# Performance work log

Measured on AMD Instinct MI355X. Metric: run time of the kernel, lower is better.

Reference implementation:

```python
import jax, jax.numpy as jnp
import numpy as np

N = 50000          # nodes
E = 400000         # edges
MUL0 = 16          # multiplicity of 0e irreps (node & message)
MUL1 = 8           # multiplicity of 1o irreps
RBF = 8
HID = 64
CUTOFF = 5.0
WNUM = MUL0*MUL0 + MUL1*MUL0 + MUL0*MUL1 + MUL1*MUL1  # 576 tp weights per edge
EPS = 1e-8
INV_SQRT3 = 1.0 / np.sqrt(3.0).astype(np.float32)
A_PATH = 1.0 / np.sqrt(float(MUL0 + MUL1))  # e3nn path normalization (fan_in = 24 for both outputs)


def _split_sv(x):
    # x: [n, 40] -> scalars [n,16], vectors [n,8,3]
    return x[:, :MUL0], x[:, MUL0:].reshape(-1, MUL1, 3)


def _irrep_norm(x):
    # RMS-normalize each irrep block separately (IrrepNorm)
    s, v = _split_sv(x)
    s_rms = jnp.sqrt(jnp.mean(s * s, axis=-1, keepdims=True) + EPS)
    v_rms = jnp.sqrt(jnp.mean(jnp.sum(v * v, axis=-1), axis=-1, keepdims=True) + EPS)
    return jnp.concatenate([s / s_rms, (v / v_rms[:, :, None]).reshape(-1, MUL1 * 3)], axis=-1)


def setup_inputs() -> dict:
    key = jax.random.key(0)
    ks = jax.random.split(key, 20)
    inp = {
        'x': jax.random.normal(ks[0], (N, MUL0 + 3 * MUL1), jnp.float32),
        'edge_src': jax.random.randint(ks[1], (E,), 0, N, jnp.int32),
        'edge_dst': jax.random.randint(ks[2], (E,), 0, N, jnp.int32),
        'edge_sh': jax.random.normal(ks[3], (E, 4), jnp.float32),
        'edge_rbf': jax.random.uniform(ks[4], (E, RBF), jnp.float32),
        'edge_len': jax.random.uniform(ks[5], (E,), jnp.float32) * CUTOFF,
        # radial MLP producing per-edge TP weights
        'w_r1': jax.random.normal(ks[6], (RBF, HID), jnp.float32) / np.sqrt(RBF),
        'b_r1': jnp.zeros((HID,), jnp.float32),
        'w_r2': jax.random.normal(ks[7], (HID, WNUM), jnp.float32) / np.sqrt(HID),
        'b_r2': jnp.zeros((WNUM,), jnp.float32),
        # edge gate MLP
        'w_g1': jax.random.normal(ks[8], (RBF, HID), jnp.float32) / np.sqrt(RBF),
        'b_g1': jnp.zeros((HID,), jnp.float32),
        'w_g2': jax.random.normal(ks[9], (HID, 1), jnp.float32) / np.sqrt(HID),
        'b_g2': jnp.zeros((1,), jnp.float32),
        # msg_linear: 16x0e+8x1o -> (16x0e scalars + 8x0e gates) + 8x1o gated
        'Wm_s': jax.random.normal(ks[10], (MUL0, MUL0 + MUL1), jnp.float32),
        'Wm_v': jax.random.normal(ks[11], (MUL1, MUL1), jnp.float32),
        # update_linear and self_linear: 16x0e+8x1o -> 16x0e+8x1o
        'Wu_s': jax.random.normal(ks[12], (MUL0, MUL0), jnp.float32),
        'Wu_v': jax.random.normal(ks[13], (MUL1, MUL1), jnp.float32),
        'Ws_s': jax.random.normal(ks[14], (MUL0, MUL0), jnp.float32),
        'Ws_v': jax.random.normal(ks[15], (MUL1, MUL1), jnp.float32),
        'res_scale': jnp.asarray(0.1, jnp.float32),
    }
    return inp


def reference(x, edge_src, edge_dst, edge_sh, edge_rbf, edge_len,
              w_r1, b_r1, w_r2, b_r2, w_g1, b_g1, w_g2, b_g2,
              Wm_s, Wm_v, Wu_s, Wu_v, Ws_s, Ws_v, res_scale):
    x_norm = _irrep_norm(x)
    xs, xv = _split_sv(x_norm)

    # per-edge TP weights from radial MLP
    w = jax.nn.silu(edge_rbf @ w_r1 + b_r1) @ w_r2 + b_r2            # [E, 576]
    o = MUL0 * MUL0
    w1 = w[:, :o].reshape(-1, MUL0, MUL0)                            # 0e x 0e -> 0e
    w2 = w[:, o:o + MUL1 * MUL0].reshape(-1, MUL1, MUL0)             # 1o x 1o -> 0e
    o += MUL1 * MUL0
    w3 = w[:, o:o + MUL0 * MUL1].reshape(-1, MUL0, MUL1)             # 0e x 1o -> 1o
    o += MUL0 * MUL1
    w4 = w[:, o:].reshape(-1, MUL1, MUL1)                            # 1o x 0e -> 1o

    # gather per-edge source features
    s_e = xs[edge_src]                                               # [E,16]
    v_e = xv[edge_src]                                               # [E,8,3]
    sh0 = edge_sh[:, :1]                                             # [E,1]
    sh1 = edge_sh[:, 1:4]                                            # [E,3]

    # fully-connected tensor product (CG for l<=1, component norm, path norm)
    m0 = A_PATH * (jnp.einsum('ei,eij->ej', s_e * sh0, w1)
                   + INV_SQRT3 * jnp.einsum('eic,ec,eij->ej', v_e, sh1, w2))   # [E,16]
    m1 = A_PATH * (jnp.einsum('ei,eij,ec->ejc', s_e, w3, sh1)
                   + jnp.einsum('eic,eij->ejc', v_e * sh0[:, :, None], w4))    # [E,8,3]

    # cutoff and sigmoid edge gate
    cw = 0.5 * (jnp.cos(jnp.pi * edge_len / CUTOFF) + 1.0) * (edge_len < CUTOFF)
    gw = jax.nn.sigmoid(jax.nn.silu(edge_rbf @ w_g1 + b_g1) @ w_g2 + b_g2)     # [E,1]
    ew = cw[:, None] * gw                                                      # [E,1]
    m0 = m0 * ew
    m1 = m1 * ew[:, :, None]

    # scatter-add into destination nodes, normalize by total edge weight
    agg0 = jax.ops.segment_sum(m0, edge_dst, num_segments=N)                   # [N,16]
    agg1 = jax.ops.segment_sum(m1.reshape(-1, MUL1 * 3), edge_dst, num_segments=N).reshape(-1, MUL1, 3)
    norm = jax.ops.segment_sum(ew, edge_dst, num_segments=N)                   # [N,1]
    norm = jnp.maximum(norm, EPS)
    agg0 = agg0 / norm
    agg1 = agg1 / norm[:, :, None]

    # msg_linear (equivariant linear, fan-in normalized)
    sc = agg0 @ Wm_s / np.sqrt(MUL0)                                           # [N,24]
    vv = jnp.einsum('nic,ij->njc', agg1, Wm_v) / np.sqrt(MUL1)                 # [N,8,3]

    # gated nonlinearity
    scal = jax.nn.silu(sc[:, :MUL0])
    gates = jax.nn.sigmoid(sc[:, MUL0:])
    vg = vv * gates[:, :, None]

    # update + self interaction, residual
    out_s = scal @ Wu_s / np.sqrt(MUL0) + xs @ Ws_s / np.sqrt(MUL0)
    out_v = (jnp.einsum('nic,ij->njc', vg, Wu_v) + jnp.einsum('nic,ij->njc', xv, Ws_v)) / np.sqrt(MUL1)
    out = jnp.concatenate([out_s, out_v.reshape(-1, MUL1 * 3)], axis=-1)
    return x + res_scale * out
```

## Files before the change

### kernel.cpp

```cpp
#include <hip/hip_runtime.h>
#include <cstdint>

#define MUL0 16
#define MUL1 8
#define NRBF 8
#define HID 64
#define WNUM 576
#define CUTOFF 5.0f
#define EPSF 1e-8f

#define INV_SQRT3 0.57735026918962576f
#define A_PATH    0.20412414523193154f
#define Q16       0.25f
#define Q8        0.35355339059327373f
#define PI_OVER_CUT 0.62831853071795865f

typedef _Float16 f16;
typedef _Float16 f16x8 __attribute__((ext_vector_type(8)));
typedef float f32x4 __attribute__((ext_vector_type(4)));

__device__ __forceinline__ float sigm(float x) { return 1.0f / (1.0f + __expf(-x)); }

extern "C" __global__ __launch_bounds__(256) void k_prep_w2t(
    const float* __restrict__ w_r2, f16* __restrict__ W2T) {
  int t = blockIdx.x * 256 + threadIdx.x;
  if (t >= HID * WNUM) return;
  int n = t >> 6, k = t & 63;
  W2T[n * 64 + k] = (f16)w_r2[k * WNUM + n];
}

extern "C" __global__ __launch_bounds__(256) void k_xnorm(
    const float* __restrict__ x, float* __restrict__ xnorm, int N) {
  int n = blockIdx.x * 256 + threadIdx.x;
  if (n >= N) return;
  const float4* xr = (const float4*)(x + (long long)n * 40);
  float4 vv[10];
#pragma unroll
  for (int i = 0; i < 10; i++) vv[i] = xr[i];
  float* f = (float*)vv;
  float ss = 0.f, vs = 0.f;
#pragma unroll
  for (int i = 0; i < 16; i++) ss += f[i] * f[i];
#pragma unroll
  for (int i = 16; i < 40; i++) vs += f[i] * f[i];
  float sr = rsqrtf(ss * (1.0f / 16.0f) + EPSF);
  float vr = rsqrtf(vs * (1.0f / 8.0f) + EPSF);
#pragma unroll
  for (int i = 0; i < 16; i++) f[i] *= sr;
#pragma unroll
  for (int i = 16; i < 40; i++) f[i] *= vr;
  float4* o = (float4*)(xnorm + (long long)n * 40);
#pragma unroll
  for (int i = 0; i < 10; i++) o[i] = vv[i];
}

extern "C" __global__ __launch_bounds__(256, 5) void k_edge(
    const float* __restrict__ xnorm, const int* __restrict__ esrc,
    const int* __restrict__ edst, const float* __restrict__ sh,
    const float* __restrict__ rbf, const float* __restrict__ elen,
    const float* __restrict__ w_r1, const float* __restrict__ b_r1,
    const float* __restrict__ w_g1, const float* __restrict__ b_g1,
    const float* __restrict__ w_g2, const float* __restrict__ b_g2,
    const float* __restrict__ b_r2, const f16* __restrict__ W2T,
    float* __restrict__ agg0, float* __restrict__ agg1,
    float* __restrict__ normb, int E) {
  __shared__ __align__(16) f16   s_H[4][16][72];
  __shared__ __align__(16) float s_sn[4][16][20];
  __shared__ __align__(16) float s_v[4][16][28];
  __shared__ __align__(16) float s_a1[4][16][12];
  __shared__ __align__(16) float s_sh[4][16][4];
  __shared__ __align__(16) float s_rbf[4][16][8];
  __shared__ float s_ew[4][16];
  __shared__ int   s_dst[4][16];

  const int t = threadIdx.x;
  const int w = t >> 6;
  const int lane = t & 63;
  const long long eb = (long long)blockIdx.x * 64 + w * 16;

  const int ge_l = lane >> 2;
  const int part = lane & 3;
  const long long ge = eb + ge_l;
  int srcn = 0;
  float4 shv = {0.f, 0.f, 0.f, 0.f};
  if (ge < E) {
    srcn = esrc[ge];
    shv = *(const float4*)&sh[ge * 4];
  }
  {
    long long gb = eb * 8 + lane;
    float r0 = (gb < (long long)E * 8) ? rbf[gb] : 0.f;
    float r1 = (gb + 64 < (long long)E * 8) ? rbf[gb + 64] : 0.f;
    (&s_rbf[w][0][0])[lane] = r0;
    (&s_rbf[w][0][0])[lane + 64] = r1;
    long long gs = eb * 4 + lane;
    (&s_sh[w][0][0])[lane] = (gs < (long long)E * 4) ? sh[gs] : 0.f;
    if (lane < 16) {
      long long g2 = eb + lane;
      s_dst[w][lane] = (g2 < E) ? edst[g2] : 0;
    }
  }
  __syncthreads();

  {
    const float* xr = xnorm + (long long)srcn * 40;
    if (part < 2) {
      float4 aLo = *(const float4*)(xr + part * 8);
      float4 aHi = *(const float4*)(xr + part * 8 + 4);
      *(float4*)&s_sn[w][ge_l][part * 8] = aLo;
      *(float4*)&s_sn[w][ge_l][part * 8 + 4] = aHi;
    } else {
      const int i0 = (part - 2) * 4;
      const float* vp = xr + 16 + i0 * 3;
      float4 v0 = *(const float4*)(vp);
      float4 v1 = *(const float4*)(vp + 4);
      float4 v2 = *(const float4*)(vp + 8);
      *(float4*)&s_v[w][ge_l][i0 * 3] = v0;
      *(float4*)&s_v[w][ge_l][i0 * 3 + 4] = v1;
      *(float4*)&s_v[w][ge_l][i0 * 3 + 8] = v2;
      float s1x = shv.y, s1y = shv.z, s1z = shv.w;
      s_a1[w][ge_l][i0]     = INV_SQRT3 * (v0.x * s1x + v0.y * s1y + v0.z * s1z);
      s_a1[w][ge_l][i0 + 1] = INV_SQRT3 * (v0.w * s1x + v1.x * s1y + v1.y * s1z);
      s_a1[w][ge_l][i0 + 2] = INV_SQRT3 * (v1.z * s1x + v1.w * s1y + v2.x * s1z);
      s_a1[w][ge_l][i0 + 3] = INV_SQRT3 * (v2.y * s1x + v2.z * s1y + v2.w * s1z);
    }
  }

  {
    float wr[8];
#pragma unroll
    for (int r = 0; r < 8; r++) wr[r] = w_r1[r * HID + lane];
    float bh = b_r1[lane];
#pragma unroll
    for (int u = 0; u < 16; u++) {
      float4 ra = *(const float4*)&s_rbf[w][u][0];
      float4 rb = *(const float4*)&s_rbf[w][u][4];
      float acc = bh + ra.x * wr[0] + ra.y * wr[1] + ra.z * wr[2] + ra.w * wr[3]
                     + rb.x * wr[4] + rb.y * wr[5] + rb.z * wr[6] + rb.w * wr[7];
      s_H[w][u][lane] = (f16)(acc * sigm(acc));
    }
  }

  {
    const int eg = lane & 15;
    const int grp = lane >> 4;
    float4 ga = *(const float4*)&s_rbf[w][eg][0];
    float4 gb = *(const float4*)&s_rbf[w][eg][4];
    float rv[8] = {ga.x, ga.y, ga.z, ga.w, gb.x, gb.y, gb.z, gb.w};
    float tt[16];
    {
      const float4 b0 = *(const float4*)&b_g1[grp * 16];
      const float4 b1 = *(const float4*)&b_g1[grp * 16 + 4];
      const float4 b2 = *(const float4*)&b_g1[grp * 16 + 8];
      const float4 b3 = *(const float4*)&b_g1[grp * 16 + 12];
      tt[0] = b0.x; tt[1] = b0.y; tt[2] = b0.z; tt[3] = b0.w;
      tt[4] = b1.x; tt[5] = b1.y; tt[6] = b1.z; tt[7] = b1.w;
      tt[8] = b2.x; tt[9] = b2.y; tt[10] = b2.z; tt[11] = b2.w;
      tt[12] = b3.x; tt[13] = b3.y; tt[14] = b3.z; tt[15] = b3.w;
    }
#pragma unroll
    for (int r = 0; r < 8; r++) {
      const float* wg = w_g1 + r * HID + grp * 16;
      float4 w0 = *(const float4*)(wg);
      float4 w1 = *(const float4*)(wg + 4);
      float4 w2 = *(const float4*)(wg + 8);
      float4 w3 = *(const float4*)(wg + 12);
      float rr = rv[r];
      tt[0] += rr * w0.x; tt[1] += rr * w0.y; tt[2] += rr * w0.z; tt[3] += rr * w0.w;
      tt[4] += rr * w1.x; tt[5] += rr * w1.y; tt[6] += rr * w1.z; tt[7] += rr * w1.w;
      tt[8] += rr * w2.x; tt[9] += rr * w2.y; tt[10] += rr * w2.z; tt[11] += rr * w2.w;
      tt[12] += rr * w3.x; tt[13] += rr * w3.y; tt[14] += rr * w3.z; tt[15] += rr * w3.w;
    }
    float gw[16];
    {
      const float4 g0 = *(const float4*)&w_g2[grp * 16];
      const float4 g1 = *(const float4*)&w_g2[grp * 16 + 4];
      const float4 g2 = *(const float4*)&w_g2[grp * 16 + 8];
      const float4 g3 = *(const float4*)&w_g2[grp * 16 + 12];
      gw[0] = g0.x; gw[1] = g0.y; gw[2] = g0.z; gw[3] = g0.w;
      gw[4] = g1.x; gw[5] = g1.y; gw[6] = g1.z; gw[7] = g1.w;
      gw[8] = g2.x; gw[9] = g2.y; gw[10] = g2.z; gw[11] = g2.w;
      gw[12] = g3.x; gw[13] = g3.y; gw[14] = g3.z; gw[15] = g3.w;
    }
    float accp = 0.f;
#pragma unroll
    for (int k = 0; k < 16; k++) accp += tt[k] * sigm(tt[k]) * gw[k];
    accp += __shfl_xor(accp, 16);
    accp += __shfl_xor(accp, 32);
    if (lane < 16) {
      long long g2e = eb + lane;
      float ew = 0.f;
      if (g2e < E) {
        float len = elen[g2e];
        float cw = (len < CUTOFF) ? 0.5f * (__cosf(PI_OVER_CUT * len) + 1.0f) : 0.f;
        ew = cw * sigm(accp + b_g2[0]);
      }
      s_ew[w][lane] = ew;
    }
  }
  __syncthreads();

  const int quad = lane >> 4;
  const int c = lane & 15;

  const f16x8 af0 = *(const f16x8*)&s_H[w][c][quad * 8];
  const f16x8 af1 = *(const f16x8*)&s_H[w][c][32 + quad * 8];

  float p1[4] = {0.f, 0.f, 0.f, 0.f};
  float p2[4] = {0.f, 0.f, 0.f, 0.f};
  float t3[4] = {0.f, 0.f, 0.f, 0.f};
  float mx[4] = {0.f, 0.f, 0.f, 0.f};
  float my[4] = {0.f, 0.f, 0.f, 0.f};
  float mz[4] = {0.f, 0.f, 0.f, 0.f};

  const f16* wb = W2T + (long long)c * 64 + quad * 8;
  const float* bp = b_r2 + c;

#pragma unroll 2
  for (int jt = 0; jt < 16; jt++) {
    f16x8 b0 = *(const f16x8*)(wb + jt * 1024);
    f16x8 b1 = *(const f16x8*)(wb + jt * 1024 + 32);
    float bias = bp[jt * 16];
    f32x4 C = {0.f, 0.f, 0.f, 0.f};
    C = __builtin_amdgcn_mfma_f32_16x16x32_f16(af0, b0, C, 0, 0, 0);
    C = __builtin_amdgcn_mfma_f32_16x16x32_f16(af1, b1, C, 0, 0, 0);
#pragma unroll
    for (int r = 0; r < 4; r++)
      p1[r] += s_sn[w][quad * 4 + r][jt] * (C[r] + bias);
  }
#pragma unroll 2
  for (int jt = 16; jt < 24; jt++) {
    f16x8 b0 = *(const f16x8*)(wb + jt * 1024);
    f16x8 b1 = *(const f16x8*)(wb + jt * 1024 + 32);
    float bias = bp[jt * 16];
    f32x4 C = {0.f, 0.f, 0.f, 0.f};
    C = __builtin_amdgcn_mfma_f32_16x16x32_f16(af0, b0, C, 0, 0, 0);
    C = __builtin_amdgcn_mfma_f32_16x16x32_f16(af1, b1, C, 0, 0, 0);
    const int i = jt - 16;
#pragma unroll
    for (int r = 0; r < 4; r++)
      p2[r] += s_a1[w][quad * 4 + r][i] * (C[r] + bias);
  }
#pragma unroll 2
  for (int jt = 24; jt < 32; jt++) {
    f16x8 b0 = *(const f16x8*)(wb + jt * 1024);
    f16x8 b1 = *(const f16x8*)(wb + jt * 1024 + 32);
    float bias = bp[jt * 16];
    f32x4 C = {0.f, 0.f, 0.f, 0.f};
    C = __builtin_amdgcn_mfma_f32_16x16x32_f16(af0, b0, C, 0, 0, 0);
    C = __builtin_amdgcn_mfma_f32_16x16x32_f16(af1, b1, C, 0, 0, 0);
    const int i = (jt - 24) * 2 + (c >> 3);
#pragma unroll
    for (int r = 0; r < 4; r++)
      t3[r] += s_sn[w][quad * 4 + r][i] * (C[r] + bias);
  }
#pragma unroll 2
  for (int jt = 32; jt < 36; jt++) {
    f16x8 b0 = *(const f16x8*)(wb + jt * 1024);
    f16x8 b1 = *(const f16x8*)(wb + jt * 1024 + 32);
    float bias = bp[jt * 16];
    f32x4 C = {0.f, 0.f, 0.f, 0.f};
    C = __builtin_amdgcn_mfma_f32_16x16x32_f16(af0, b0, C, 0, 0, 0);
    C = __builtin_amdgcn_mfma_f32_16x16x32_f16(af1, b1, C, 0, 0, 0);
    const int i = (jt - 32) * 2 + (c >> 3);
#pragma unroll
    for (int r = 0; r < 4; r++) {
      float wvv = C[r] + bias;
      mx[r] += s_v[w][quad * 4 + r][3 * i] * wvv;
      my[r] += s_v[w][quad * 4 + r][3 * i + 1] * wvv;
      mz[r] += s_v[w][quad * 4 + r][3 * i + 2] * wvv;
    }
  }

#pragma unroll
  for (int r = 0; r < 4; r++) {
    t3[r] += __shfl_xor(t3[r], 8);
    mx[r] += __shfl_xor(mx[r], 8);
    my[r] += __shfl_xor(my[r], 8);
    mz[r] += __shfl_xor(mz[r], 8);
  }

#pragma unroll
  for (int r = 0; r < 4; r++) {
    const int e = quad * 4 + r;
    float ew = s_ew[w][e];
    float sc = A_PATH * ew;
    int dst = s_dst[w][e];
    float sh0 = s_sh[w][e][0];
    atomicAdd(&agg0[(long long)dst * 16 + c], (sh0 * p1[r] + p2[r]) * sc);
    if (c < 8) {
      float t3v = t3[r] * sc;
      float scs = sc * sh0;
      float ox = t3v * s_sh[w][e][1] + mx[r] * scs;
      float oy = t3v * s_sh[w][e][2] + my[r] * scs;
      float oz = t3v * s_sh[w][e][3] + mz[r] * scs;
      long long b = (long long)dst * 24 + (long long)c * 3;
      atomicAdd(&agg1[b], ox);
      atomicAdd(&agg1[b + 1], oy);
      atomicAdd(&agg1[b + 2], oz);
    } else if (c == 8) {
      atomicAdd(&normb[dst], ew);
    }
  }
}

extern "C" __global__ __launch_bounds__(256) void k_node(
    const float* __restrict__ x, const float* __restrict__ xnorm,
    const float* __restrict__ agg0, const float* __restrict__ agg1,
    const float* __restrict__ normb, const float* __restrict__ Wm_s,
    const float* __restrict__ Wm_v, const float* __restrict__ Wu_s,
    const float* __restrict__ Wu_v, const float* __restrict__ Ws_s,
    const float* __restrict__ Ws_v, const float* __restrict__ res_scale_p,
    float* __restrict__ out, int N) {
  __shared__ float sWms[384];
  __shared__ float sWmv[64];
  __shared__ float sWus[256];
  __shared__ float sWuv[64];
  __shared__ float sWss[256];
  __shared__ float sWsv[64];
  int t = threadIdx.x;
  for (int i = t; i < 384; i += 256) sWms[i] = Wm_s[i];
  if (t < 64) sWmv[t] = Wm_v[t];
  sWus[t] = Wu_s[t];
  if (t < 64) sWuv[t] = Wu_v[t];
  sWss[t] = Ws_s[t];
  if (t < 64) sWsv[t] = Ws_v[t];
  __syncthreads();
  int n = blockIdx.x * 256 + t;
  if (n >= N) return;

  float inv = 1.0f / fmaxf(normb[n], EPSF);
  float4 a04[4], a14[6];
  {
    const float4* p = (const float4*)(agg0 + (long long)n * 16);
#pragma unroll
    for (int i = 0; i < 4; i++) a04[i] = p[i];
    const float4* q = (const float4*)(agg1 + (long long)n * 24);
#pragma unroll
    for (int i = 0; i < 6; i++) a14[i] = q[i];
  }
  float* a0 = (float*)a04;
  float* a1 = (float*)a14;
#pragma unroll
  for (int i = 0; i < 16; i++) a0[i] *= inv;
#pragma unroll
  for (int i = 0; i < 24; i++) a1[i] *= inv;

  float scal[16], gate[8];
#pragma unroll
  for (int jj = 0; jj < 24; jj++) {
    float acc = 0.f;
#pragma unroll
    for (int i = 0; i < 16; i++) acc += a0[i] * sWms[i * 24 + jj];
    acc *= Q16;
    if (jj < 16) scal[jj] = acc * sigm(acc);
    else gate[jj - 16] = sigm(acc);
  }
  float vg[24];
#pragma unroll
  for (int j = 0; j < 8; j++) {
    float g = gate[j];
#pragma unroll
    for (int cc = 0; cc < 3; cc++) {
      float acc = 0.f;
#pragma unroll
      for (int i = 0; i < 8; i++) acc += a1[i * 3 + cc] * sWmv[i * 8 + j];
      vg[j * 3 + cc] = acc * Q8 * g;
    }
  }
  float4 xn4[10], xo4[10];
  {
    const float4* p = (const float4*)(xnorm + (long long)n * 40);
    const float4* q = (const float4*)(x + (long long)n * 40);
#pragma unroll
    for (int i = 0; i < 10; i++) { xn4[i] = p[i]; xo4[i] = q[i]; }
  }
  const float* xn = (const float*)xn4;
  const float* xo = (const float*)xo4;
  float rs = res_scale_p[0];

  float4 ob[10];
  float* ov = (float*)ob;
#pragma unroll
  for (int j = 0; j < 16; j++) {
    float acc = 0.f, acc2 = 0.f;
#pragma unroll
    for (int i = 0; i < 16; i++) {
      acc += scal[i] * sWus[i * 16 + j];
      acc2 += xn[i] * sWss[i * 16 + j];
    }
    ov[j] = xo[j] + rs * ((acc + acc2) * Q16);
  }
#pragma unroll
  for (int j = 0; j < 8; j++) {
#pragma unroll
    for (int cc = 0; cc < 3; cc++) {
      float acc = 0.f;
#pragma unroll
      for (int i = 0; i < 8; i++)
        acc += vg[i * 3 + cc] * sWuv[i * 8 + j] + xn[16 + i * 3 + cc] * sWsv[i * 8 + j];
      ov[16 + j * 3 + cc] = xo[16 + j * 3 + cc] + rs * (acc * Q8);
    }
  }
  float4* po = (float4*)(out + (long long)n * 40);
#pragma unroll
  for (int i = 0; i < 10; i++) po[i] = ob[i];
}

extern "C" void kernel_launch(void* const* d_in, const int* in_sizes, int n_in,
                              void* d_out, int out_size, void* d_ws, size_t ws_size,
                              hipStream_t stream) {
  const float* x = (const float*)d_in[0];
  const int* esrc = (const int*)d_in[1];
  const int* edst = (const int*)d_in[2];
  const float* sh = (const float*)d_in[3];
  const float* rbf = (const float*)d_in[4];
  const float* elen = (const float*)d_in[5];
  const float* w_r1 = (const float*)d_in[6];
  const float* b_r1 = (const float*)d_in[7];
  const float* w_r2 = (const float*)d_in[8];
  const float* b_r2 = (const float*)d_in[9];
  const float* w_g1 = (const float*)d_in[10];
  const float* b_g1 = (const float*)d_in[11];
  const float* w_g2 = (const float*)d_in[12];
  const float* b_g2 = (const float*)d_in[13];
  const float* Wm_s = (const float*)d_in[14];
  const float* Wm_v = (const float*)d_in[15];
  const float* Wu_s = (const float*)d_in[16];
  const float* Wu_v = (const float*)d_in[17];
  const float* Ws_s = (const float*)d_in[18];
  const float* Ws_v = (const float*)d_in[19];
  const float* res_scale = (const float*)d_in[20];

  const int N = in_sizes[0] / 40;
  const int E = in_sizes[1];

  char* ws = (char*)d_ws;
  size_t off = 0;
  float* xnorm = (float*)(ws + off); off += (size_t)N * 40 * sizeof(float);
  off = (off + 255) & ~(size_t)255;
  float* agg0 = (float*)(ws + off); off += (size_t)N * 16 * sizeof(float);
  float* agg1 = (float*)(ws + off); off += (size_t)N * 24 * sizeof(float);
  float* normb = (float*)(ws + off); off += (size_t)N * sizeof(float);
  off = (off + 255) & ~(size_t)255;
  f16* W2T = (f16*)(ws + off); off += (size_t)WNUM * 64 * sizeof(f16);

  hipMemsetAsync(agg0, 0, (size_t)N * 41 * sizeof(float), stream);

  k_prep_w2t<<<(HID * WNUM + 255) / 256, 256, 0, stream>>>(w_r2, W2T);
  k_xnorm<<<(N + 255) / 256, 256, 0, stream>>>(x, xnorm, N);

  int nblk = (E + 63) / 64;
  k_edge<<<nblk, 256, 0, stream>>>(xnorm, esrc, edst, sh, rbf, elen, w_r1, b_r1,
                                   w_g1, b_g1, w_g2, b_g2, b_r2, W2T, agg0, agg1,
                                   normb, E);

  k_node<<<(N + 255) / 256, 256, 0, stream>>>(x, xnorm, agg0, agg1, normb, Wm_s,
                                              Wm_v, Wu_s, Wu_v, Ws_s, Ws_v,
                                              res_scale, (float*)d_out, N);
}
```

Baseline: 404.2 us.

## Counting-sort edges by destination and merge same-destination atomics in edge kernel

Adds a per-call counting sort of edges by destination (histogram, prefix scan, atomic scatter of edge attributes). The edge kernel then reads the sorted arrays and accumulates consecutive contributions to the same node in registers before issuing atomics. This is meant to cut atomic traffic and contention and to improve locality of the scatter-add. In exchange it adds several extra kernels and a full copy of edge data each call. k_xnorm and k_node also move to 64-thread blocks.

```diff
diff --git a/kernel.cpp b/kernel.cpp
--- a/kernel.cpp
+++ b/kernel.cpp
@@ -29,9 +29,9 @@
   W2T[n * 64 + k] = (f16)w_r2[k * WNUM + n];
 }
 
-extern "C" __global__ __launch_bounds__(256) void k_xnorm(
+extern "C" __global__ __launch_bounds__(64) void k_xnorm(
     const float* __restrict__ x, float* __restrict__ xnorm, int N) {
-  int n = blockIdx.x * 256 + threadIdx.x;
+  int n = blockIdx.x * 64 + threadIdx.x;
   if (n >= N) return;
   const float4* xr = (const float4*)(x + (long long)n * 40);
   float4 vv[10];
@@ -52,6 +52,75 @@
   float4* o = (float4*)(xnorm + (long long)n * 40);
 #pragma unroll
   for (int i = 0; i < 10; i++) o[i] = vv[i];
+}
+
+extern "C" __global__ __launch_bounds__(256) void k_hist(
+    const int* __restrict__ edst, int* __restrict__ hist, int E) {
+  int e = blockIdx.x * 256 + threadIdx.x;
+  if (e < E) atomicAdd(&hist[edst[e]], 1);
+}
+
+extern "C" __global__ __launch_bounds__(256) void k_scan1(
+    const int* __restrict__ hist, int* __restrict__ iscan,
+    int* __restrict__ bsum, int N) {
+  __shared__ int sm[256];
+  int i = blockIdx.x * 256 + threadIdx.x;
+  int t = threadIdx.x;
+  sm[t] = (i < N) ? hist[i] : 0;
+  __syncthreads();
+#pragma unroll
+  for (int d = 1; d < 256; d <<= 1) {
+    int add = (t >= d) ? sm[t - d] : 0;
+    __syncthreads();
+    sm[t] += add;
+    __syncthreads();
+  }
+  if (i < N) iscan[i] = sm[t];
+  if (t == 255) bsum[blockIdx.x] = sm[255];
+}
+
+extern "C" __global__ __launch_bounds__(256) void k_scan2(
+    int* __restrict__ bsum, int nb) {
+  __shared__ int sm[256];
+  int t = threadIdx.x;
+  sm[t] = (t < nb) ? bsum[t] : 0;
+  __syncthreads();
+#pragma unroll
+  for (int d = 1; d < 256; d <<= 1) {
+    int add = (t >= d) ? sm[t - d] : 0;
+    __syncthreads();
+    sm[t] += add;
+    __syncthreads();
+  }
+  if (t < nb) bsum[t] = sm[t];
+}
+
+extern "C" __global__ __launch_bounds__(256) void k_scan3(
+    const int* __restrict__ hist, const int* __restrict__ iscan,
+    const int* __restrict__ bsum, int* __restrict__ cursor, int N) {
+  int i = blockIdx.x * 256 + threadIdx.x;
+  if (i >= N) return;
+  int base = blockIdx.x ? bsum[blockIdx.x - 1] : 0;
+  cursor[i] = iscan[i] - hist[i] + base;
+}
+
+extern "C" __global__ __launch_bounds__(256) void k_scatter(
+    const int* __restrict__ esrc, const int* __restrict__ edst,
+    const float* __restrict__ sh, const float* __restrict__ rbf,
+    const float* __restrict__ elen, int* __restrict__ cursor,
+    int* __restrict__ esrc_s, int* __restrict__ edst_s,
+    float* __restrict__ sh_s, float* __restrict__ rbf_s,
+    float* __restrict__ elen_s, int E) {
+  int e = blockIdx.x * 256 + threadIdx.x;
+  if (e >= E) return;
+  int d = edst[e];
+  int p = atomicAdd(&cursor[d], 1);
+  esrc_s[p] = esrc[e];
+  edst_s[p] = d;
+  elen_s[p] = elen[e];
+  *(float4*)&sh_s[(long long)p * 4] = *(const float4*)&sh[(long long)e * 4];
+  *(float4*)&rbf_s[(long long)p * 8] = *(const float4*)&rbf[(long long)e * 8];
+  *(float4*)&rbf_s[(long long)p * 8 + 4] = *(const float4*)&rbf[(long long)e * 8 + 4];
 }
 
 extern "C" __global__ __launch_bounds__(256, 5) void k_edge(
@@ -280,31 +349,53 @@
     mz[r] += __shfl_xor(mz[r], 8);
   }
 
-#pragma unroll
-  for (int r = 0; r < 4; r++) {
-    const int e = quad * 4 + r;
-    float ew = s_ew[w][e];
-    float sc = A_PATH * ew;
-    int dst = s_dst[w][e];
-    float sh0 = s_sh[w][e][0];
-    atomicAdd(&agg0[(long long)dst * 16 + c], (sh0 * p1[r] + p2[r]) * sc);
+  {
+    int cur = s_dst[w][quad * 4];
+    float acc0 = 0.f, a1x = 0.f, a1y = 0.f, a1z = 0.f, nacc = 0.f;
+#pragma unroll
+    for (int r = 0; r < 4; r++) {
+      const int e = quad * 4 + r;
+      const int dst = s_dst[w][e];
+      if (dst != cur) {
+        atomicAdd(&agg0[(long long)cur * 16 + c], acc0);
+        if (c < 8) {
+          long long b = (long long)cur * 24 + (long long)c * 3;
+          atomicAdd(&agg1[b], a1x);
+          atomicAdd(&agg1[b + 1], a1y);
+          atomicAdd(&agg1[b + 2], a1z);
+        } else if (c == 8) {
+          atomicAdd(&normb[cur], nacc);
+        }
+        acc0 = a1x = a1y = a1z = nacc = 0.f;
+        cur = dst;
+      }
+      float ew = s_ew[w][e];
+      float sc = A_PATH * ew;
+      float sh0 = s_sh[w][e][0];
+      acc0 += (sh0 * p1[r] + p2[r]) * sc;
+      if (c < 8) {
+        float t3v = t3[r] * sc;
+        float scs = sc * sh0;
+        a1x += t3v * s_sh[w][e][1] + mx[r] * scs;
+        a1y += t3v * s_sh[w][e][2] + my[r] * scs;
+        a1z += t3v * s_sh[w][e][3] + mz[r] * scs;
+      } else if (c == 8) {
+        nacc += ew;
+      }
+    }
+    atomicAdd(&agg0[(long long)cur * 16 + c], acc0);
     if (c < 8) {
-      float t3v = t3[r] * sc;
-      float scs = sc * sh0;
-      float ox = t3v * s_sh[w][e][1] + mx[r] * scs;
-      float oy = t3v * s_sh[w][e][2] + my[r] * scs;
-      float oz = t3v * s_sh[w][e][3] + mz[r] * scs;
-      long long b = (long long)dst * 24 + (long long)c * 3;
-      atomicAdd(&agg1[b], ox);
-      atomicAdd(&agg1[b + 1], oy);
-      atomicAdd(&agg1[b + 2], oz);
+      long long b = (long long)cur * 24 + (long long)c * 3;
+      atomicAdd(&agg1[b], a1x);
+      atomicAdd(&agg1[b + 1], a1y);
+      atomicAdd(&agg1[b + 2], a1z);
     } else if (c == 8) {
-      atomicAdd(&normb[dst], ew);
-    }
-  }
-}
-
-extern "C" __global__ __launch_bounds__(256) void k_node(
+      atomicAdd(&normb[cur], nacc);
+    }
+  }
+}
+
+extern "C" __global__ __launch_bounds__(64) void k_node(
     const float* __restrict__ x, const float* __restrict__ xnorm,
     const float* __restrict__ agg0, const float* __restrict__ agg1,
     const float* __restrict__ normb, const float* __restrict__ Wm_s,
@@ -319,14 +410,14 @@
   __shared__ float sWss[256];
   __shared__ float sWsv[64];
   int t = threadIdx.x;
-  for (int i = t; i < 384; i += 256) sWms[i] = Wm_s[i];
-  if (t < 64) sWmv[t] = Wm_v[t];
-  sWus[t] = Wu_s[t];
-  if (t < 64) sWuv[t] = Wu_v[t];
-  sWss[t] = Ws_s[t];
-  if (t < 64) sWsv[t] = Ws_v[t];
+  for (int i = t; i < 384; i += 64) sWms[i] = Wm_s[i];
+  sWmv[t] = Wm_v[t];
+  for (int i = t; i < 256; i += 64) sWus[i] = Wu_s[i];
+  sWuv[t] = Wu_v[t];
+  for (int i = t; i < 256; i += 64) sWss[i] = Ws_s[i];
+  sWsv[t] = Ws_v[t];
   __syncthreads();
-  int n = blockIdx.x * 256 + t;
+  int n = blockIdx.x * 64 + t;
   if (n >= N) return;
 
   float inv = 1.0f / fmaxf(normb[n], EPSF);
@@ -444,18 +535,41 @@
   float* normb = (float*)(ws + off); off += (size_t)N * sizeof(float);
   off = (off + 255) & ~(size_t)255;
   f16* W2T = (f16*)(ws + off); off += (size_t)WNUM * 64 * sizeof(f16);
+  off = (off + 255) & ~(size_t)255;
+  int* hist   = (int*)(ws + off); off += (size_t)N * sizeof(int);
+  int* iscan  = (int*)(ws + off); off += (size_t)N * sizeof(int);
+  int* cursor = (int*)(ws + off); off += (size_t)N * sizeof(int);
+  int* bsum   = (int*)(ws + off); off += 256 * sizeof(int);
+  off = (off + 255) & ~(size_t)255;
+  int* esrc_s = (int*)(ws + off); off += (size_t)E * sizeof(int);
+  int* edst_s = (int*)(ws + off); off += (size_t)E * sizeof(int);
+  float* elen_s = (float*)(ws + off); off += (size_t)E * sizeof(float);
+  off = (off + 255) & ~(size_t)255;
+  float* sh_s  = (float*)(ws + off); off += (size_t)E * 4 * sizeof(float);
+  float* rbf_s = (float*)(ws + off); off += (size_t)E * 8 * sizeof(float);
 
   hipMemsetAsync(agg0, 0, (size_t)N * 41 * sizeof(float), stream);
+  hipMemsetAsync(hist, 0, (size_t)N * sizeof(int), stream);
+
+  const int nbE = (E + 255) / 256;
+  const int nbN = (N + 255) / 256;
+
+  k_hist<<<nbE, 256, 0, stream>>>(edst, hist, E);
+  k_scan1<<<nbN, 256, 0, stream>>>(hist, iscan, bsum, N);
+  k_scan2<<<1, 256, 0, stream>>>(bsum, nbN);
+  k_scan3<<<nbN, 256, 0, stream>>>(hist, iscan, bsum, cursor, N);
+  k_scatter<<<nbE, 256, 0, stream>>>(esrc, edst, sh, rbf, elen, cursor,
+                                     esrc_s, edst_s, sh_s, rbf_s, elen_s, E);
 
   k_prep_w2t<<<(HID * WNUM + 255) / 256, 256, 0, stream>>>(w_r2, W2T);
-  k_xnorm<<<(N + 255) / 256, 256, 0, stream>>>(x, xnorm, N);
+  k_xnorm<<<(N + 63) / 64, 64, 0, stream>>>(x, xnorm, N);
 
   int nblk = (E + 63) / 64;
-  k_edge<<<nblk, 256, 0, stream>>>(xnorm, esrc, edst, sh, rbf, elen, w_r1, b_r1,
-                                   w_g1, b_g1, w_g2, b_g2, b_r2, W2T, agg0, agg1,
-                                   normb, E);
-
-  k_node<<<(N + 255) / 256, 256, 0, stream>>>(x, xnorm, agg0, agg1, normb, Wm_s,
-                                              Wm_v, Wu_s, Wu_v, Ws_s, Ws_v,
-                                              res_scale, (float*)d_out, N);
-}
+  k_edge<<<nblk, 256, 0, stream>>>(xnorm, esrc_s, edst_s, sh_s, rbf_s, elen_s,
+                                   w_r1, b_r1, w_g1, b_g1, w_g2, b_g2, b_r2,
+                                   W2T, agg0, agg1, normb, E);
+
+  k_node<<<(N + 63) / 64, 64, 0, stream>>>(x, xnorm, agg0, agg1, normb, Wm_s,
+                                           Wm_v, Wu_s, Wu_v, Ws_s, Ws_v,
+                                           res_scale, (float*)d_out, N);
+}
```

Measured after the change: 448.2 us. 10.9% more time.
